# Kernel optimization log

Hardware: AMD Instinct MI355X
Metric: run time of the kernel (lower is better)

Reference implementation:

```python
import jax, jax.numpy as jnp
import numpy as np

K_IN, K_OUT, K_STATE = 32, 32, 1024
BATCH, SEQ = 64, 512


def setup_inputs() -> dict:
    key = jax.random.key(0)
    ks = jax.random.split(key, 10)
    stdv = 1.0 / np.sqrt(K_STATE)
    u = lambda k, shape: jax.random.uniform(k, shape, jnp.float32, -stdv, stdv)
    return {
        "inputs": jax.random.normal(ks[0], (BATCH, SEQ, K_IN), jnp.float32),
        "state0": jnp.zeros((K_STATE,), jnp.float32),
        "W_e": u(ks[1], (K_STATE, K_IN)),
        "b_e": u(ks[2], (K_STATE,)),
        "W_ih": u(ks[3], (3 * K_STATE, K_STATE)),
        "b_ih": u(ks[4], (3 * K_STATE,)),
        "W_hh": u(ks[5], (3 * K_STATE, K_STATE)),
        "b_hh": u(ks[6], (3 * K_STATE,)),
        "W_ly": u(ks[7], (K_OUT, K_STATE)),
    }


def reference(inputs, state0, W_e, b_e, W_ih, b_ih, W_hh, b_hh, W_ly):
    # inputs: (B, T, k_in). interpol='constant' => x_half/x_full are unused by GRUCell.
    B, T, _ = inputs.shape
    H = W_hh.shape[1]
    # expand_input: tanh(Linear(k_in -> k_state)), batched over all timesteps
    xe = jnp.tanh(jnp.einsum('btk,hk->bth', inputs, W_e) + b_e)  # (B,T,H)
    # precompute input-side GRU gate projections in one big matmul
    xp = jnp.einsum('bth,gh->btg', xe, W_ih) + b_ih  # (B,T,3H)
    h0 = jnp.broadcast_to(state0, (B, H))

    def step(h, xp_t):
        gh = h @ W_hh.T + b_hh  # (B,3H)
        xr, xz, xn = jnp.split(xp_t, 3, axis=-1)
        hr, hz, hn = jnp.split(gh, 3, axis=-1)
        r = jax.nn.sigmoid(xr + hr)
        z = jax.nn.sigmoid(xz + hz)
        n = jnp.tanh(xn + r * hn)
        h_new = (1.0 - z) * n + z * h
        return h_new, h_new

    _, hs = jax.lax.scan(step, h0, jnp.swapaxes(xp, 0, 1))  # hs: (T,B,H)
    states = jnp.swapaxes(hs, 0, 1)  # (B,T,H)
    outputs = jnp.einsum('bth,oh->bto', states, W_ly)  # (B,T,k_out)
    return outputs, states
```

## Files before the change

### kernel.cpp

```cpp
#include <hip/hip_runtime.h>
#include <hip/hip_bf16.h>
#include <stdint.h>

typedef short short8 __attribute__((ext_vector_type(8)));
typedef float f32x4 __attribute__((ext_vector_type(4)));
typedef unsigned short u16;

__device__ __forceinline__ float bf2f(u16 b){ unsigned u = ((unsigned)b) << 16; float f; __builtin_memcpy(&f, &u, 4); return f; }
__device__ __forceinline__ u16 f2bf(float f){ unsigned u; __builtin_memcpy(&u, &f, 4); u = (u + 0x7fffu + ((u >> 16) & 1u)) >> 16; return (u16)u; }
__device__ __forceinline__ float sigm(float x){ return 1.f / (1.f + __expf(-x)); }
__device__ __forceinline__ float tanh_(float x){ float e = __expf(2.f * x); return 1.f - 2.f / (e + 1.f); }

__device__ __forceinline__ short8 ld_cohx4(const u16* p){
  short8 d;
  asm volatile("global_load_dwordx4 %0, %1, off sc0 sc1" : "=v"(d) : "v"(p) : "memory");
  return d;
}
__device__ __forceinline__ int ld_coh_u32(const int* p){
  int d;
  asm volatile("global_load_dword %0, %1, off sc0 sc1" : "=v"(d) : "v"(p) : "memory");
  return d;
}
__device__ __forceinline__ void st_coh_u16(u16* p, u16 v){
  asm volatile("global_store_short %0, %1, off sc0 sc1" :: "v"(p), "v"(v) : "memory");
}
__device__ __forceinline__ void st_coh_u32(int* p, int v){
  asm volatile("global_store_dword %0, %1, off sc0 sc1" :: "v"(p), "v"(v) : "memory");
}
__device__ __forceinline__ void wait_vm0(){ asm volatile("s_waitcnt vmcnt(0)" ::: "memory"); }

__global__ __launch_bounds__(256) void k_init(const float* __restrict__ Wih, const float* __restrict__ Whh,
                                              const float* __restrict__ Wly, const float* __restrict__ s0,
                                              u16* __restrict__ Wihb, u16* __restrict__ Whhb,
                                              u16* __restrict__ Wlyb, u16* __restrict__ hslab,
                                              int* __restrict__ flags)
{
  int i = blockIdx.x * 256 + threadIdx.x;
  int n = 3072 * 1024;
  for (int idx = i; idx < n; idx += gridDim.x * 256){
    Wihb[idx] = f2bf(Wih[idx]);
    Whhb[idx] = f2bf(Whh[idx]);
  }
  if (i < 32 * 1024) Wlyb[i] = f2bf(Wly[i]);
  if (i < 65536){
    int k = ((i >> 8) & 63) * 16 + (i & 15);
    hslab[65536 + i] = f2bf(s0[k]);
  }
  if (i < 4 * 512 * 64) flags[i] = 0;
}

__global__ __launch_bounds__(256) void k_xe(const float* __restrict__ inp, const float* __restrict__ We,
                                            const float* __restrict__ be, u16* __restrict__ xe)
{
  __shared__ float si[64][32];
  size_t m0 = (size_t)blockIdx.x * 64;
  int tid = threadIdx.x;
  for (int i = tid; i < 2048; i += 256)
    si[i >> 5][i & 31] = inp[m0 * 32 + i];
  __syncthreads();
  #pragma unroll
  for (int jj = 0; jj < 4; ++jj){
    int j = jj * 256 + tid;
    f32x4 wr[8];
    #pragma unroll
    for (int q = 0; q < 8; ++q)
      wr[q] = *(const f32x4*)(We + (size_t)j * 32 + q * 4);
    float bias = be[j];
    for (int mi = 0; mi < 64; ++mi){
      float acc = bias;
      #pragma unroll
      for (int q = 0; q < 8; ++q){
        f32x4 x = *(const f32x4*)(&si[mi][q * 4]);
        acc += x[0]*wr[q][0] + x[1]*wr[q][1] + x[2]*wr[q][2] + x[3]*wr[q][3];
      }
      xe[(m0 + mi) * 1024 + j] = f2bf(tanh_(acc));
    }
  }
}

__global__ __launch_bounds__(256) void k_xp(const u16* __restrict__ A, const u16* __restrict__ Bw,
                                            const float* __restrict__ bias, u16* __restrict__ C)
{
  __shared__ u16 As[128 * 32];
  __shared__ u16 Bs[128 * 32];
  int tid = threadIdx.x;
  int lane = tid & 63, wv = tid >> 6;
  int wr = wv >> 1, wc = wv & 1;
  int l15 = lane & 15, l4 = lane >> 4;
  int bid = blockIdx.x;
  int mb = bid / 24, nb = bid % 24;
  int m0 = mb * 128, n0 = nb * 128;

  int srow = tid >> 2;
  int sslot = tid & 3;
  int wb0 = srow * 64 + ((sslot ^ ((srow >> 1) & 3)) * 16);
  int swz = (l15 >> 1) & 3;
  int rb_ = l15 * 64 + ((l4 ^ swz) * 16);

  f32x4 acc[4][4] = {};
  const u16* Aptr = A + (size_t)m0 * 1024;
  const u16* Bptr = Bw + (size_t)n0 * 1024;

  for (int k0 = 0; k0 < 1024; k0 += 32){
    short8 va0 = *(const short8*)(Aptr + (size_t)srow * 1024 + k0 + sslot * 8);
    short8 va1 = *(const short8*)(Aptr + (size_t)(srow + 64) * 1024 + k0 + sslot * 8);
    short8 vb0 = *(const short8*)(Bptr + (size_t)srow * 1024 + k0 + sslot * 8);
    short8 vb1 = *(const short8*)(Bptr + (size_t)(srow + 64) * 1024 + k0 + sslot * 8);
    __syncthreads();
    *(short8*)((char*)As + wb0)        = va0;
    *(short8*)((char*)As + wb0 + 4096) = va1;
    *(short8*)((char*)Bs + wb0)        = vb0;
    *(short8*)((char*)Bs + wb0 + 4096) = vb1;
    __syncthreads();
    short8 af[4], bf[4];
    #pragma unroll
    for (int i = 0; i < 4; ++i){
      af[i] = *(const short8*)((const char*)As + (wr * 64 + i * 16) * 64 + rb_);
      bf[i] = *(const short8*)((const char*)Bs + (wc * 64 + i * 16) * 64 + rb_);
    }
    #pragma unroll
    for (int i = 0; i < 4; ++i)
      #pragma unroll
      for (int j = 0; j < 4; ++j)
        acc[i][j] = __builtin_amdgcn_mfma_f32_16x16x32_bf16(af[i], bf[j], acc[i][j], 0, 0, 0);
  }
  #pragma unroll
  for (int j = 0; j < 4; ++j){
    int n = n0 + wc * 64 + j * 16 + l15;
    float bv = bias[n];
    #pragma unroll
    for (int i = 0; i < 4; ++i){
      int mrow = m0 + wr * 64 + i * 16 + l4 * 4;
      #pragma unroll
      for (int r = 0; r < 4; ++r)
        C[(size_t)(mrow + r) * 3072 + n] = f2bf(acc[i][j][r] + bv);
    }
  }
}

__global__ __launch_bounds__(256, 1) void k_rec(const u16* __restrict__ Whhb, const float* __restrict__ bhh,
                                                const u16* __restrict__ xpb, const float* __restrict__ s0,
                                                u16* __restrict__ hslab, float* __restrict__ states,
                                                int* __restrict__ flags)
{
  int w = blockIdx.x;
  int g = w & 3;
  int s = w >> 2;
  int jb = s * 16;
  int tid = threadIdx.x, lane = tid & 63, wv = tid >> 6;
  int l15 = lane & 15, l4 = lane >> 4;

  short8 wreg[3][8];
  #pragma unroll
  for (int gt = 0; gt < 3; ++gt){
    const u16* wp = Whhb + (size_t)(gt * 1024 + jb + l15) * 1024 + wv * 256 + l4 * 8;
    #pragma unroll
    for (int ks = 0; ks < 8; ++ks)
      wreg[gt][ks] = *(const short8*)(wp + ks * 32);
  }
  float bb0 = bhh[jb + l15], bb1 = bhh[1024 + jb + l15], bb2 = bhh[2048 + jb + l15];
  float hreg[4];
  { float v = s0[jb + l15]; hreg[0] = hreg[1] = hreg[2] = hreg[3] = v; }

  __shared__ f32x4 part[3][3][64];

  for (int t = 0; t < 512; ++t){
    u16 xq[12];
    if (wv == 0){
      #pragma unroll
      for (int gt = 0; gt < 3; ++gt)
        #pragma unroll
        for (int r = 0; r < 4; ++r){
          int b = g * 16 + l4 * 4 + r;
          xq[gt * 4 + r] = xpb[((size_t)b * 512 + t) * 3072 + gt * 1024 + jb + l15];
        }
    }
    if (t > 0){
      const int* fp_ = flags + ((size_t)g * 512 + (t - 1)) * 64 + wv * 16 + l15;
      while (true){
        int v = ld_coh_u32(fp_);
        wait_vm0();
        if (__all(v != 0)) break;
        __builtin_amdgcn_s_sleep(1);
      }
      __builtin_amdgcn_sched_barrier(0);
    }
    int rbuf = (t & 1) ^ 1;
    const char* hs = (const char*)hslab + (((size_t)rbuf * 4 + g) * 64 + wv * 16) * 512;
    const char* hl = hs + l15 * 32 + (l4 & 1) * 16;
    short8 af[8];
    #pragma unroll
    for (int ks = 0; ks < 8; ++ks)
      af[ks] = ld_cohx4((const u16*)(hl + (ks * 2 + (l4 >> 1)) * 512));
    wait_vm0();
    __builtin_amdgcn_sched_barrier(0);
    f32x4 a0 = {}, a1 = {}, a2 = {};
    #pragma unroll
    for (int ks = 0; ks < 8; ++ks){
      a0 = __builtin_amdgcn_mfma_f32_16x16x32_bf16(af[ks], wreg[0][ks], a0, 0, 0, 0);
      a1 = __builtin_amdgcn_mfma_f32_16x16x32_bf16(af[ks], wreg[1][ks], a1, 0, 0, 0);
      a2 = __builtin_amdgcn_mfma_f32_16x16x32_bf16(af[ks], wreg[2][ks], a2, 0, 0, 0);
    }
    if (wv){
      part[wv - 1][0][lane] = a0;
      part[wv - 1][1][lane] = a1;
      part[wv - 1][2][lane] = a2;
    }
    __syncthreads();
    if (wv == 0){
      f32x4 g0 = a0 + part[0][0][lane] + part[1][0][lane] + part[2][0][lane];
      f32x4 g1 = a1 + part[0][1][lane] + part[1][1][lane] + part[2][1][lane];
      f32x4 g2 = a2 + part[0][2][lane] + part[1][2][lane] + part[2][2][lane];
      int wb = t & 1;
      float hn_[4];
      #pragma unroll
      for (int r = 0; r < 4; ++r){
        float rr = sigm(bf2f(xq[r])      + g0[r] + bb0);
        float zz = sigm(bf2f(xq[4 + r])  + g1[r] + bb1);
        float nn = tanh_(bf2f(xq[8 + r]) + rr * (g2[r] + bb2));
        hn_[r] = (1.f - zz) * nn + zz * hreg[r];
        hreg[r] = hn_[r];
      }
      u16* hw = hslab + (((size_t)wb * 4 + g) * 64 + s) * 256;
      #pragma unroll
      for (int r = 0; r < 4; ++r)
        st_coh_u16(hw + (l4 * 4 + r) * 16 + l15, f2bf(hn_[r]));
      wait_vm0();
      if (lane == 0)
        st_coh_u32(flags + ((size_t)g * 512 + t) * 64 + s, 1);
      #pragma unroll
      for (int r = 0; r < 4; ++r)
        states[((size_t)(g * 16 + l4 * 4 + r) * 512 + t) * 1024 + jb + l15] = hn_[r];
    }
  }
}

__global__ __launch_bounds__(256) void k_out(const float* __restrict__ st, const u16* __restrict__ Wlyb,
                                             float* __restrict__ out)
{
  int tid = threadIdx.x, lane = tid & 63, wv = tid >> 6;
  int l15 = lane & 15, l4 = lane >> 4;
  size_t m0 = (size_t)blockIdx.x * 256;
  f32x4 acc[4][2] = {};
  for (int kc = 0; kc < 4; ++kc){
    short8 bfr[2][8];
    #pragma unroll
    for (int nt = 0; nt < 2; ++nt){
      const u16* bp = Wlyb + (size_t)(nt * 16 + l15) * 1024 + kc * 256 + l4 * 8;
      #pragma unroll
      for (int ks = 0; ks < 8; ++ks)
        bfr[nt][ks] = *(const short8*)(bp + ks * 32);
    }
    #pragma unroll
    for (int mt = 0; mt < 4; ++mt){
      const float* sp = st + (m0 + wv * 64 + mt * 16 + l15) * 1024 + kc * 256 + l4 * 8;
      #pragma unroll
      for (int ks = 0; ks < 8; ++ks){
        f32x4 p0 = *(const f32x4*)(sp + ks * 32);
        f32x4 p1 = *(const f32x4*)(sp + ks * 32 + 4);
        short8 a;
        a[0] = (short)f2bf(p0[0]); a[1] = (short)f2bf(p0[1]); a[2] = (short)f2bf(p0[2]); a[3] = (short)f2bf(p0[3]);
        a[4] = (short)f2bf(p1[0]); a[5] = (short)f2bf(p1[1]); a[6] = (short)f2bf(p1[2]); a[7] = (short)f2bf(p1[3]);
        acc[mt][0] = __builtin_amdgcn_mfma_f32_16x16x32_bf16(a, bfr[0][ks], acc[mt][0], 0, 0, 0);
        acc[mt][1] = __builtin_amdgcn_mfma_f32_16x16x32_bf16(a, bfr[1][ks], acc[mt][1], 0, 0, 0);
      }
    }
  }
  #pragma unroll
  for (int mt = 0; mt < 4; ++mt)
    #pragma unroll
    for (int nt = 0; nt < 2; ++nt)
      #pragma unroll
      for (int r = 0; r < 4; ++r)
        out[(m0 + wv * 64 + mt * 16 + l4 * 4 + r) * 32 + nt * 16 + l15] = acc[mt][nt][r];
}

extern "C" void kernel_launch(void* const* d_in, const int* in_sizes, int n_in,
                              void* d_out, int out_size, void* d_ws, size_t ws_size,
                              hipStream_t stream)
{
  const float* inputs = (const float*)d_in[0];
  const float* s0     = (const float*)d_in[1];
  const float* We     = (const float*)d_in[2];
  const float* be     = (const float*)d_in[3];
  const float* Wih    = (const float*)d_in[4];
  const float* bih    = (const float*)d_in[5];
  const float* Whh    = (const float*)d_in[6];
  const float* bhh    = (const float*)d_in[7];
  const float* Wly    = (const float*)d_in[8];

  float* out    = (float*)d_out;
  float* states = out + (size_t)64 * 512 * 32;

  char* ws = (char*)d_ws;
  u16* xe   = (u16*)ws;  ws += (size_t)32768 * 1024 * 2;
  u16* xpb  = (u16*)ws;  ws += (size_t)32768 * 3072 * 2;
  u16* Wihb = (u16*)ws;  ws += (size_t)3072 * 1024 * 2;
  u16* Whhb = (u16*)ws;  ws += (size_t)3072 * 1024 * 2;
  u16* Wlyb = (u16*)ws;  ws += (size_t)32 * 1024 * 2;
  u16* hslab= (u16*)ws;  ws += (size_t)2 * 4 * 64 * 256 * 2;
  int* flags= (int*)ws;  ws += (size_t)4 * 512 * 64 * 4;

  k_init<<<dim3(4096), dim3(256), 0, stream>>>(Wih, Whh, Wly, s0, Wihb, Whhb, Wlyb, hslab, flags);
  k_xe<<<dim3(512), dim3(256), 0, stream>>>(inputs, We, be, xe);
  k_xp<<<dim3(6144), dim3(256), 0, stream>>>(xe, Wihb, bih, xpb);

  void* args[] = { (void*)&Whhb, (void*)&bhh, (void*)&xpb, (void*)&s0, (void*)&hslab, (void*)&states, (void*)&flags };
  hipError_t e = hipLaunchCooperativeKernel((const void*)k_rec, dim3(256), dim3(256), args, 0, stream);
  if (e != hipSuccess){
    (void)hipGetLastError();
    k_rec<<<dim3(256), dim3(256), 0, stream>>>(Whhb, bhh, xpb, s0, hslab, states, flags);
  }
  k_out<<<dim3(128), dim3(256), 0, stream>>>(states, Wlyb, out);
}
```

Before: 3.239 ms.

## Use direct global-to-LDS loads in xp GEMM and simplify output projection to fp32

```diff
diff --git a/kernel.cpp b/kernel.cpp
--- a/kernel.cpp
+++ b/kernel.cpp
@@ -30,10 +30,9 @@
 __device__ __forceinline__ void wait_vm0(){ asm volatile("s_waitcnt vmcnt(0)" ::: "memory"); }
 
 __global__ __launch_bounds__(256) void k_init(const float* __restrict__ Wih, const float* __restrict__ Whh,
-                                              const float* __restrict__ Wly, const float* __restrict__ s0,
+                                              const float* __restrict__ s0,
                                               u16* __restrict__ Wihb, u16* __restrict__ Whhb,
-                                              u16* __restrict__ Wlyb, u16* __restrict__ hslab,
-                                              int* __restrict__ flags)
+                                              u16* __restrict__ hslab, int* __restrict__ flags)
 {
   int i = blockIdx.x * 256 + threadIdx.x;
   int n = 3072 * 1024;
@@ -41,7 +40,6 @@
     Wihb[idx] = f2bf(Wih[idx]);
     Whhb[idx] = f2bf(Whh[idx]);
   }
-  if (i < 32 * 1024) Wlyb[i] = f2bf(Wly[i]);
   if (i < 65536){
     int k = ((i >> 8) & 63) * 16 + (i & 15);
     hslab[65536 + i] = f2bf(s0[k]);
@@ -83,40 +81,30 @@
 {
   __shared__ u16 As[128 * 32];
   __shared__ u16 Bs[128 * 32];
-  int tid = threadIdx.x;
-  int lane = tid & 63, wv = tid >> 6;
+  int tid = threadIdx.x, lane = tid & 63, wv = tid >> 6;
   int wr = wv >> 1, wc = wv & 1;
   int l15 = lane & 15, l4 = lane >> 4;
   int bid = blockIdx.x;
   int mb = bid / 24, nb = bid % 24;
   int m0 = mb * 128, n0 = nb * 128;
 
-  int srow = tid >> 2;
-  int sslot = tid & 3;
-  int wb0 = srow * 64 + ((sslot ^ ((srow >> 1) & 3)) * 16);
-  int swz = (l15 >> 1) & 3;
-  int rb_ = l15 * 64 + ((l4 ^ swz) * 16);
+  int srow = lane >> 2, skk = (lane & 3) * 8;
+  const u16* Ab = A + ((size_t)m0 + wv * 32 + srow) * 1024 + skk;
+  const u16* Bb = Bw + ((size_t)n0 + wv * 32 + srow) * 1024 + skk;
 
   f32x4 acc[4][4] = {};
-  const u16* Aptr = A + (size_t)m0 * 1024;
-  const u16* Bptr = Bw + (size_t)n0 * 1024;
-
   for (int k0 = 0; k0 < 1024; k0 += 32){
-    short8 va0 = *(const short8*)(Aptr + (size_t)srow * 1024 + k0 + sslot * 8);
-    short8 va1 = *(const short8*)(Aptr + (size_t)(srow + 64) * 1024 + k0 + sslot * 8);
-    short8 vb0 = *(const short8*)(Bptr + (size_t)srow * 1024 + k0 + sslot * 8);
-    short8 vb1 = *(const short8*)(Bptr + (size_t)(srow + 64) * 1024 + k0 + sslot * 8);
     __syncthreads();
-    *(short8*)((char*)As + wb0)        = va0;
-    *(short8*)((char*)As + wb0 + 4096) = va1;
-    *(short8*)((char*)Bs + wb0)        = vb0;
-    *(short8*)((char*)Bs + wb0 + 4096) = vb1;
+    __builtin_amdgcn_global_load_lds(Ab + k0,              &As[(wv * 2)     * 512], 16, 0, 0);
+    __builtin_amdgcn_global_load_lds(Ab + k0 + 16 * 1024,  &As[(wv * 2 + 1) * 512], 16, 0, 0);
+    __builtin_amdgcn_global_load_lds(Bb + k0,              &Bs[(wv * 2)     * 512], 16, 0, 0);
+    __builtin_amdgcn_global_load_lds(Bb + k0 + 16 * 1024,  &Bs[(wv * 2 + 1) * 512], 16, 0, 0);
     __syncthreads();
     short8 af[4], bf[4];
     #pragma unroll
     for (int i = 0; i < 4; ++i){
-      af[i] = *(const short8*)((const char*)As + (wr * 64 + i * 16) * 64 + rb_);
-      bf[i] = *(const short8*)((const char*)Bs + (wc * 64 + i * 16) * 64 + rb_);
+      af[i] = *(const short8*)(As + (size_t)(wr * 64 + i * 16 + l15) * 32 + l4 * 8);
+      bf[i] = *(const short8*)(Bs + (size_t)(wc * 64 + i * 16 + l15) * 32 + l4 * 8);
     }
     #pragma unroll
     for (int i = 0; i < 4; ++i)
@@ -235,44 +223,25 @@
   }
 }
 
-__global__ __launch_bounds__(256) void k_out(const float* __restrict__ st, const u16* __restrict__ Wlyb,
+__global__ __launch_bounds__(256) void k_out(const float* __restrict__ st, const float* __restrict__ Wly,
                                              float* __restrict__ out)
 {
-  int tid = threadIdx.x, lane = tid & 63, wv = tid >> 6;
-  int l15 = lane & 15, l4 = lane >> 4;
-  size_t m0 = (size_t)blockIdx.x * 256;
-  f32x4 acc[4][2] = {};
-  for (int kc = 0; kc < 4; ++kc){
-    short8 bfr[2][8];
-    #pragma unroll
-    for (int nt = 0; nt < 2; ++nt){
-      const u16* bp = Wlyb + (size_t)(nt * 16 + l15) * 1024 + kc * 256 + l4 * 8;
-      #pragma unroll
-      for (int ks = 0; ks < 8; ++ks)
-        bfr[nt][ks] = *(const short8*)(bp + ks * 32);
-    }
-    #pragma unroll
-    for (int mt = 0; mt < 4; ++mt){
-      const float* sp = st + (m0 + wv * 64 + mt * 16 + l15) * 1024 + kc * 256 + l4 * 8;
-      #pragma unroll
-      for (int ks = 0; ks < 8; ++ks){
-        f32x4 p0 = *(const f32x4*)(sp + ks * 32);
-        f32x4 p1 = *(const f32x4*)(sp + ks * 32 + 4);
-        short8 a;
-        a[0] = (short)f2bf(p0[0]); a[1] = (short)f2bf(p0[1]); a[2] = (short)f2bf(p0[2]); a[3] = (short)f2bf(p0[3]);
-        a[4] = (short)f2bf(p1[0]); a[5] = (short)f2bf(p1[1]); a[6] = (short)f2bf(p1[2]); a[7] = (short)f2bf(p1[3]);
-        acc[mt][0] = __builtin_amdgcn_mfma_f32_16x16x32_bf16(a, bfr[0][ks], acc[mt][0], 0, 0, 0);
-        acc[mt][1] = __builtin_amdgcn_mfma_f32_16x16x32_bf16(a, bfr[1][ks], acc[mt][1], 0, 0, 0);
-      }
-    }
-  }
-  #pragma unroll
-  for (int mt = 0; mt < 4; ++mt)
-    #pragma unroll
-    for (int nt = 0; nt < 2; ++nt)
-      #pragma unroll
-      for (int r = 0; r < 4; ++r)
-        out[(m0 + wv * 64 + mt * 16 + l4 * 4 + r) * 32 + nt * 16 + l15] = acc[mt][nt][r];
+  __shared__ float srow[8][1024];
+  size_t m0 = (size_t)blockIdx.x * 8;
+  int tid = threadIdx.x;
+  for (int i = tid; i < 8 * 1024; i += 256)
+    srow[i >> 10][i & 1023] = st[(m0 + (i >> 10)) * 1024 + (i & 1023)];
+  __syncthreads();
+  int mi = tid >> 5, o = tid & 31;
+  const float* wp = Wly + (size_t)o * 1024;
+  float acc = 0.f;
+  #pragma unroll 4
+  for (int k = 0; k < 1024; k += 4){
+    f32x4 w = *(const f32x4*)(wp + k);
+    f32x4 x = *(const f32x4*)(&srow[mi][k]);
+    acc += x[0]*w[0] + x[1]*w[1] + x[2]*w[2] + x[3]*w[3];
+  }
+  out[(m0 + mi) * 32 + o] = acc;
 }
 
 extern "C" void kernel_launch(void* const* d_in, const int* in_sizes, int n_in,
@@ -293,23 +262,23 @@
   float* states = out + (size_t)64 * 512 * 32;
 
   char* ws = (char*)d_ws;
-  u16* xe   = (u16*)ws;  ws += (size_t)32768 * 1024 * 2;
-  u16* xpb  = (u16*)ws;  ws += (size_t)32768 * 3072 * 2;
-  u16* Wihb = (u16*)ws;  ws += (size_t)3072 * 1024 * 2;
-  u16* Whhb = (u16*)ws;  ws += (size_t)3072 * 1024 * 2;
-  u16* Wlyb = (u16*)ws;  ws += (size_t)32 * 1024 * 2;
-  u16* hslab= (u16*)ws;  ws += (size_t)2 * 4 * 64 * 256 * 2;
-  int* flags= (int*)ws;  ws += (size_t)4 * 512 * 64 * 4;
-
-  k_init<<<dim3(4096), dim3(256), 0, stream>>>(Wih, Whh, Wly, s0, Wihb, Whhb, Wlyb, hslab, flags);
+  u16* xe    = (u16*)ws;  ws += (size_t)32768 * 1024 * 2;
+  u16* xpb   = (u16*)ws;  ws += (size_t)32768 * 3072 * 2;
+  u16* Wihb  = (u16*)ws;  ws += (size_t)3072 * 1024 * 2;
+  u16* Whhb  = (u16*)ws;  ws += (size_t)3072 * 1024 * 2;
+  u16* hslab = (u16*)ws;  ws += (size_t)2 * 4 * 64 * 256 * 2;
+  int* flags = (int*)ws;  ws += (size_t)4 * 512 * 64 * 4;
+
+  k_init<<<dim3(4096), dim3(256), 0, stream>>>(Wih, Whh, s0, Wihb, Whhb, hslab, flags);
   k_xe<<<dim3(512), dim3(256), 0, stream>>>(inputs, We, be, xe);
   k_xp<<<dim3(6144), dim3(256), 0, stream>>>(xe, Wihb, bih, xpb);
 
-  void* args[] = { (void*)&Whhb, (void*)&bhh, (void*)&xpb, (void*)&s0, (void*)&hslab, (void*)&states, (void*)&flags };
+  void* args[] = { (void*)&Whhb, (void*)&bhh, (void*)&xpb, (void*)&s0,
+                   (void*)&hslab, (void*)&states, (void*)&flags };
   hipError_t e = hipLaunchCooperativeKernel((const void*)k_rec, dim3(256), dim3(256), args, 0, stream);
   if (e != hipSuccess){
     (void)hipGetLastError();
     k_rec<<<dim3(256), dim3(256), 0, stream>>>(Whhb, bhh, xpb, s0, hslab, states, flags);
   }
-  k_out<<<dim3(128), dim3(256), 0, stream>>>(states, Wlyb, out);
-}
+  k_out<<<dim3(4096), dim3(256), 0, stream>>>(states, Wly, out);
+}
```

After: 3.594 ms. 1.11x slower.
